# Kernel optimization log

Hardware: AMD Instinct MI355X
Metric: run time of the kernel (lower is better)

Reference implementation:

```python
import jax, jax.numpy as jnp
import numpy as np

KERNEL_MUL = 2.0
KERNEL_NUM = 5


def setup_inputs() -> dict:
    key = jax.random.key(0)
    k1, k2 = jax.random.split(key)
    source = jax.random.normal(k1, (4096, 256), dtype=jnp.float32)
    target = jax.random.normal(k2, (4096, 256), dtype=jnp.float32)
    return {"source": source, "target": target}


def reference(source, target):
    B = source.shape[0]
    total = jnp.concatenate([source, target], axis=0)  # [2N, D]
    n = total.shape[0]
    # Pairwise squared L2 distances via ||a||^2 + ||b||^2 - 2 a.b (same math,
    # avoids the O(n^2 * D) expanded intermediate of the torch code).
    sq = jnp.sum(total * total, axis=-1)  # [2N]
    L2 = sq[:, None] + sq[None, :] - 2.0 * (total @ total.T)  # [2N, 2N]
    L2 = jnp.maximum(L2, 0.0)  # exact distances are non-negative
    # bandwidth uses L2_distance.data in torch -> stop_gradient here
    bandwidth = jax.lax.stop_gradient(jnp.sum(L2)) / (n * n - n)
    bandwidth = bandwidth / (KERNEL_MUL ** (KERNEL_NUM // 2))
    kernels = jnp.zeros_like(L2)
    for i in range(KERNEL_NUM):
        bw = bandwidth * (KERNEL_MUL ** i) + 1e-9
        kernels = kernels + jnp.exp(-L2 / bw)
    xx = jnp.mean(kernels[:B, :B])
    yy = jnp.mean(kernels[B:, B:])
    xy = jnp.mean(kernels[:B, B:])
    yx = jnp.mean(kernels[B:, :B])
    loss = xx + yy - xy - yx  # == mean(XX + YY - XY - YX) since blocks are BxB
    return (loss, jnp.max(L2), xx, yy, xy, yx)
```

## Files before the change

kernel.cpp:

```cpp
#include <hip/hip_runtime.h>
#include <math.h>


constexpr int NTOT  = 8192;
constexpr int BHALF = 4096;
constexpr int DIM   = 256;
constexpr int BM    = 128;

typedef __attribute__((ext_vector_type(8))) short bf16x8;
typedef __attribute__((ext_vector_type(4))) float f32x4;

#define GLOAD_LDS16(gp, lp)                                                      \
    __builtin_amdgcn_global_load_lds(                                            \
        (__attribute__((address_space(1))) const void*)(gp),                     \
        (__attribute__((address_space(3))) void*)(lp), 16, 0, 0)


__device__ __forceinline__ int swz(int row, int byteInRow) {
    return (row * 128 + byteInRow) ^ ((row & 7) << 4);
}

__device__ __forceinline__ unsigned short rne_bf16(float f) {
    unsigned u = __float_as_uint(f);
    return (unsigned short)((u + 0x7fffu + ((u >> 16) & 1u)) >> 16);
}

__global__ __launch_bounds__(256) void prep_kernel(
        const float* __restrict__ src, const float* __restrict__ tgt,
        float* __restrict__ sq, float* __restrict__ colpart,
        unsigned short* __restrict__ hi) {
    __shared__ float cs[4][256];
    const int t = threadIdx.x;
    const int w = t >> 6, l = t & 63;
    const int seg = l >> 4;
    const int b8  = (l * 8) & 127;
    float c0 = 0.f, c1 = 0.f, c2 = 0.f, c3 = 0.f;

#pragma unroll
    for (int it = 0; it < 8; ++it) {
        const int row = blockIdx.x * 32 + w * 8 + it;
        const float* p = (row < BHALF) ? src + (size_t)row * DIM
                                       : tgt + (size_t)(row - BHALF) * DIM;
        float4 v = reinterpret_cast<const float4*>(p)[l];
        float s = v.x * v.x + v.y * v.y + v.z * v.z + v.w * v.w;
#pragma unroll
        for (int off = 32; off; off >>= 1) s += __shfl_down(s, off);
        if (l == 0) sq[row] = s;
        c0 += v.x; c1 += v.y; c2 += v.z; c3 += v.w;

        unsigned hp0 = (unsigned)rne_bf16(v.x) | ((unsigned)rne_bf16(v.y) << 16);
        unsigned hp1 = (unsigned)rne_bf16(v.z) | ((unsigned)rne_bf16(v.w) << 16);
        const size_t byteoff = (size_t)row * 512 + seg * 128 + (b8 ^ ((row & 7) << 4));
        *reinterpret_cast<uint2*>((char*)hi + byteoff) = make_uint2(hp0, hp1);
    }

    cs[w][l * 4 + 0] = c0; cs[w][l * 4 + 1] = c1;
    cs[w][l * 4 + 2] = c2; cs[w][l * 4 + 3] = c3;
    __syncthreads();
    colpart[blockIdx.x * 256 + t] = cs[0][t] + cs[1][t] + cs[2][t] + cs[3][t];
}

__global__ void bw_kernel(const float* __restrict__ sq,
                          const float* __restrict__ colpart,
                          float* __restrict__ bwp) {
    __shared__ double red[256];
    int t = threadIdx.x;
    double s = 0.0;
    for (int i = t; i < NTOT; i += 256) s += (double)sq[i];
    red[t] = s; __syncthreads();
    for (int off = 128; off; off >>= 1) {
        if (t < off) red[t] += red[t + off];
        __syncthreads();
    }
    double S1 = red[0];
    __syncthreads();
    double v = 0.0;
    for (int b = 0; b < 256; ++b) v += (double)colpart[b * 256 + t];
    red[t] = v * v; __syncthreads();
    for (int off = 128; off; off >>= 1) {
        if (t < off) red[t] += red[t + off];
        __syncthreads();
    }
    if (t == 0) {
        double V2 = red[0];
        const double n = (double)NTOT;
        double sumL2 = 2.0 * n * S1 - 2.0 * V2;
        *bwp = (float)(sumL2 / (n * n - n) / 4.0);
    }
}

__global__ __launch_bounds__(256) void gram_kernel(
        const unsigned short* __restrict__ hi,
        const float* __restrict__ sq, const float* __restrict__ bwp,
        double* __restrict__ qsum, int* __restrict__ maxBits) {
    const int tb = blockIdx.x;
    const int id = (tb & 7) * 260 + (tb >> 3);
    int k = 2079 - id;
    int u = (int)((sqrt((double)(8 * k + 1)) - 1.0) * 0.5);
    while ((u + 1) * (u + 2) / 2 <= k) ++u;
    while (u * (u + 1) / 2 > k) --u;
    const int by = 63 - u;
    const int bx = 63 - (k - u * (u + 1) / 2);
    const bool diag = (bx == by);

    __shared__ alignas(16) char ldsA[BM * 128];
    __shared__ alignas(16) char ldsB[BM * 128];
    __shared__ double sred[4];
    __shared__ float  mred[4];

    const int i0 = by * BM;
    const int j0 = bx * BM;
    const char* Ahi = (const char*)hi + (size_t)i0 * 512;
    const char* Bhi = (const char*)hi + (size_t)j0 * 512;

    const int t    = threadIdx.x;
    const int lane = t & 63;
    const int w    = t >> 6;
    const int wr   = w >> 1;
    const int wc   = w & 1;
    const int lrow = lane & 15;

    f32x4 acc[4][4] = {};

    for (int seg = 0; seg < 4; ++seg) {
#pragma unroll
        for (int it = 0; it < 4; ++it) {
            const int chunk = it * 4 + w;
            const int o     = chunk * 1024 + lane * 16;
            const int row   = o >> 7;
            const size_t srcoff = (size_t)row * 512 + seg * 128 + (o & 127);
            GLOAD_LDS16(Ahi + srcoff, ldsA + chunk * 1024);
            if (!diag) GLOAD_LDS16(Bhi + srcoff, ldsB + chunk * 1024);
        }
        __syncthreads();

        const char* bbuf = diag ? ldsA : ldsB;
#pragma unroll
        for (int ks = 0; ks < 2; ++ks) {
            const int kb = ks * 64 + (lane >> 4) * 16;
            bf16x8 a[4], b[4];
#pragma unroll
            for (int mt = 0; mt < 4; ++mt)
                a[mt] = *reinterpret_cast<const bf16x8*>(
                    ldsA + swz(wr * 64 + mt * 16 + lrow, kb));
#pragma unroll
            for (int nt = 0; nt < 4; ++nt)
                b[nt] = *reinterpret_cast<const bf16x8*>(
                    bbuf + swz(wc * 64 + nt * 16 + lrow, kb));
#pragma unroll
            for (int mt = 0; mt < 4; ++mt)
#pragma unroll
                for (int nt = 0; nt < 4; ++nt)
                    acc[mt][nt] = __builtin_amdgcn_mfma_f32_16x16x32_bf16(
                        a[mt], b[nt], acc[mt][nt], 0, 0, 0);
        }
        __syncthreads();
    }

    const float bw  = *bwp;
    const float ic4 = -1.44269504088896340736f / (bw * 16.0f + 1e-9f);

    float m = 0.0f;
    float ksum = 0.0f;
    const int rbase = i0 + wr * 64 + (lane >> 4) * 4;
    const int cbase = j0 + wc * 64 + lrow;
    float sb[4];
#pragma unroll
    for (int nt = 0; nt < 4; ++nt) sb[nt] = sq[cbase + nt * 16];
#pragma unroll
    for (int mt = 0; mt < 4; ++mt) {
        float sa[4];
#pragma unroll
        for (int r = 0; r < 4; ++r) sa[r] = sq[rbase + mt * 16 + r];
#pragma unroll
        for (int nt = 0; nt < 4; ++nt)
#pragma unroll
            for (int r = 0; r < 4; ++r) {
                float l2 = fmaxf(fmaf(-2.0f, acc[mt][nt][r], sa[r] + sb[nt]), 0.0f);
                m = fmaxf(m, l2);
                float e1  = exp2f(l2 * ic4);
                float e2  = e1 * e1;
                float e4  = e2 * e2;
                float e8  = e4 * e4;
                float e16 = e8 * e8;
                ksum += (e1 + e2) + (e4 + e8) + e16;
            }
    }

    double s = (double)ksum;
#pragma unroll
    for (int off = 32; off; off >>= 1) {
        s += __shfl_down(s, off);
        m  = fmaxf(m, __shfl_down(m, off));
    }
    if ((t & 63) == 0) { sred[w] = s; mred[w] = m; }
    __syncthreads();
    if (t == 0) {
        double st = sred[0] + sred[1] + sred[2] + sred[3];
        float  mt = fmaxf(fmaxf(mred[0], mred[1]), fmaxf(mred[2], mred[3]));
        atomicMax(maxBits, __float_as_int(mt));
        const int q  = (((i0 >= BHALF) ? 2 : 0) | ((j0 >= BHALF) ? 1 : 0));
        const int qT = (((j0 >= BHALF) ? 2 : 0) | ((i0 >= BHALF) ? 1 : 0));
        if (diag) {
            atomicAdd(&qsum[q], st);
        } else if (q == qT) {
            atomicAdd(&qsum[q], 2.0 * st);
        } else {
            atomicAdd(&qsum[q],  st);
            atomicAdd(&qsum[qT], st);
        }
    }
}

__global__ void final_kernel(const double* __restrict__ qsum,
                             const int* __restrict__ maxBits,
                             float* __restrict__ out) {
    const double denom = (double)BHALF * (double)BHALF;
    const double xx = qsum[0] / denom;
    const double xy = qsum[1] / denom;
    const double yx = qsum[2] / denom;
    const double yy = qsum[3] / denom;
    out[0] = (float)(xx + yy - xy - yx);
    out[1] = __int_as_float(*maxBits);
    out[2] = (float)xx;
    out[3] = (float)yy;
    out[4] = (float)xy;
    out[5] = (float)yx;
}

extern "C" void kernel_launch(void* const* d_in, const int* in_sizes, int n_in,
                              void* d_out, int out_size, void* d_ws, size_t ws_size,
                              hipStream_t stream) {
    const float* src = (const float*)d_in[0];
    const float* tgt = (const float*)d_in[1];
    float* out = (float*)d_out;

    double* qsum    = (double*)d_ws;
    int*    maxB    = (int*)   ((char*)d_ws + 32);
    float*  bwp     = (float*) ((char*)d_ws + 36);
    float*  sq      = (float*) ((char*)d_ws + 2112);
    unsigned short* hi = (unsigned short*)((char*)d_ws + 36864);
    float*  colpart = (float*) ((char*)d_ws + 36864 + (size_t)NTOT * DIM * 2);

    hipMemsetAsync(d_ws, 0, 64, stream);

    prep_kernel<<<NTOT / 32, 256, 0, stream>>>(src, tgt, sq, colpart, hi);
    bw_kernel<<<1, 256, 0, stream>>>(sq, colpart, bwp);
    gram_kernel<<<2080, 256, 0, stream>>>(hi, sq, bwp, qsum, maxB);
    final_kernel<<<1, 1, 0, stream>>>(qsum, maxB, out);
}
```

Measured before the change: 158.9 us.

## Fold bandwidth and final reductions into last-block epilogues; double-buffer gram LDS

The separate bandwidth and finalize kernels are removed. The last prep block (found by an atomic counter) computes the bandwidth, and the last gram block writes the outputs, which saves two kernel launches and their serialization gaps. The gram kernel also double-buffers its LDS tiles so the next K segment is loaded while the current one feeds MFMA. The cost is twice the LDS use, which may lower occupancy, plus extra atomics and fences.

```diff
diff --git a/kernel.cpp b/kernel.cpp
--- a/kernel.cpp
+++ b/kernel.cpp
@@ -28,13 +28,18 @@
 __global__ __launch_bounds__(256) void prep_kernel(
         const float* __restrict__ src, const float* __restrict__ tgt,
         float* __restrict__ sq, float* __restrict__ colpart,
-        unsigned short* __restrict__ hi) {
-    __shared__ float cs[4][256];
+        float* __restrict__ sqpart, unsigned short* __restrict__ hi,
+        int* __restrict__ prepCounter, float* __restrict__ bwp) {
+    __shared__ float  cs[4][256];
+    __shared__ float  sblk[256];
+    __shared__ double red[256];
+    __shared__ unsigned lastFlag;
     const int t = threadIdx.x;
     const int w = t >> 6, l = t & 63;
     const int seg = l >> 4;
     const int b8  = (l * 8) & 127;
     float c0 = 0.f, c1 = 0.f, c2 = 0.f, c3 = 0.f;
+    float sqacc = 0.f;
 
 #pragma unroll
     for (int it = 0; it < 8; ++it) {
@@ -43,6 +48,7 @@
                                        : tgt + (size_t)(row - BHALF) * DIM;
         float4 v = reinterpret_cast<const float4*>(p)[l];
         float s = v.x * v.x + v.y * v.y + v.z * v.z + v.w * v.w;
+        sqacc += s;
 #pragma unroll
         for (int off = 32; off; off >>= 1) s += __shfl_down(s, off);
         if (l == 0) sq[row] = s;
@@ -56,43 +62,47 @@
 
     cs[w][l * 4 + 0] = c0; cs[w][l * 4 + 1] = c1;
     cs[w][l * 4 + 2] = c2; cs[w][l * 4 + 3] = c3;
+    sblk[t] = sqacc;
     __syncthreads();
     colpart[blockIdx.x * 256 + t] = cs[0][t] + cs[1][t] + cs[2][t] + cs[3][t];
-}
-
-__global__ void bw_kernel(const float* __restrict__ sq,
-                          const float* __restrict__ colpart,
-                          float* __restrict__ bwp) {
-    __shared__ double red[256];
-    int t = threadIdx.x;
-    double s = 0.0;
-    for (int i = t; i < NTOT; i += 256) s += (double)sq[i];
-    red[t] = s; __syncthreads();
     for (int off = 128; off; off >>= 1) {
-        if (t < off) red[t] += red[t + off];
+        if (t < off) sblk[t] += sblk[t + off];
         __syncthreads();
     }
-    double S1 = red[0];
-    __syncthreads();
-    double v = 0.0;
-    for (int b = 0; b < 256; ++b) v += (double)colpart[b * 256 + t];
-    red[t] = v * v; __syncthreads();
-    for (int off = 128; off; off >>= 1) {
-        if (t < off) red[t] += red[t + off];
-        __syncthreads();
-    }
-    if (t == 0) {
-        double V2 = red[0];
-        const double n = (double)NTOT;
-        double sumL2 = 2.0 * n * S1 - 2.0 * V2;
-        *bwp = (float)(sumL2 / (n * n - n) / 4.0);
+    if (t == 0) sqpart[blockIdx.x] = sblk[0];
+
+    __threadfence();
+    if (t == 0) lastFlag = (atomicAdd(prepCounter, 1) == (NTOT / 32 - 1)) ? 1u : 0u;
+    __syncthreads();
+    if (lastFlag) {
+        __threadfence();
+        double v = 0.0;
+        for (int b = 0; b < 256; ++b) v += (double)colpart[b * 256 + t];
+        red[t] = v * v; __syncthreads();
+        for (int off = 128; off; off >>= 1) {
+            if (t < off) red[t] += red[t + off];
+            __syncthreads();
+        }
+        double V2 = red[0]; __syncthreads();
+        red[t] = (double)sqpart[t]; __syncthreads();
+        for (int off = 128; off; off >>= 1) {
+            if (t < off) red[t] += red[t + off];
+            __syncthreads();
+        }
+        if (t == 0) {
+            double S1 = red[0];
+            const double n = (double)NTOT;
+            double sumL2 = 2.0 * n * S1 - 2.0 * V2;
+            *bwp = (float)(sumL2 / (n * n - n) / 4.0);
+        }
     }
 }
 
 __global__ __launch_bounds__(256) void gram_kernel(
         const unsigned short* __restrict__ hi,
         const float* __restrict__ sq, const float* __restrict__ bwp,
-        double* __restrict__ qsum, int* __restrict__ maxBits) {
+        double* __restrict__ qsum, int* __restrict__ maxBits,
+        int* __restrict__ gramCounter, float* __restrict__ out) {
     const int tb = blockIdx.x;
     const int id = (tb & 7) * 260 + (tb >> 3);
     int k = 2079 - id;
@@ -103,10 +113,11 @@
     const int bx = 63 - (k - u * (u + 1) / 2);
     const bool diag = (bx == by);
 
-    __shared__ alignas(16) char ldsA[BM * 128];
-    __shared__ alignas(16) char ldsB[BM * 128];
+    __shared__ alignas(16) char ldsA[2][BM * 128];
+    __shared__ alignas(16) char ldsB[2][BM * 128];
     __shared__ double sred[4];
     __shared__ float  mred[4];
+    __shared__ unsigned lastFlag;
 
     const int i0 = by * BM;
     const int j0 = bx * BM;
@@ -122,19 +133,26 @@
 
     f32x4 acc[4][4] = {};
 
-    for (int seg = 0; seg < 4; ++seg) {
+    auto STAGE = [&](int seg, int buf) {
 #pragma unroll
         for (int it = 0; it < 4; ++it) {
             const int chunk = it * 4 + w;
             const int o     = chunk * 1024 + lane * 16;
             const int row   = o >> 7;
             const size_t srcoff = (size_t)row * 512 + seg * 128 + (o & 127);
-            GLOAD_LDS16(Ahi + srcoff, ldsA + chunk * 1024);
-            if (!diag) GLOAD_LDS16(Bhi + srcoff, ldsB + chunk * 1024);
-        }
-        __syncthreads();
-
-        const char* bbuf = diag ? ldsA : ldsB;
+            GLOAD_LDS16(Ahi + srcoff, &ldsA[buf][chunk * 1024]);
+            if (!diag) GLOAD_LDS16(Bhi + srcoff, &ldsB[buf][chunk * 1024]);
+        }
+    };
+
+    STAGE(0, 0);
+    __syncthreads();
+
+#pragma unroll
+    for (int seg = 0; seg < 4; ++seg) {
+        if (seg < 3) STAGE(seg + 1, (seg + 1) & 1);
+        const char* abuf = ldsA[seg & 1];
+        const char* bbuf = diag ? ldsA[seg & 1] : ldsB[seg & 1];
 #pragma unroll
         for (int ks = 0; ks < 2; ++ks) {
             const int kb = ks * 64 + (lane >> 4) * 16;
@@ -142,7 +160,7 @@
 #pragma unroll
             for (int mt = 0; mt < 4; ++mt)
                 a[mt] = *reinterpret_cast<const bf16x8*>(
-                    ldsA + swz(wr * 64 + mt * 16 + lrow, kb));
+                    abuf + swz(wr * 64 + mt * 16 + lrow, kb));
 #pragma unroll
             for (int nt = 0; nt < 4; ++nt)
                 b[nt] = *reinterpret_cast<const bf16x8*>(
@@ -209,23 +227,26 @@
             atomicAdd(&qsum[q],  st);
             atomicAdd(&qsum[qT], st);
         }
-    }
-}
-
-__global__ void final_kernel(const double* __restrict__ qsum,
-                             const int* __restrict__ maxBits,
-                             float* __restrict__ out) {
-    const double denom = (double)BHALF * (double)BHALF;
-    const double xx = qsum[0] / denom;
-    const double xy = qsum[1] / denom;
-    const double yx = qsum[2] / denom;
-    const double yy = qsum[3] / denom;
-    out[0] = (float)(xx + yy - xy - yx);
-    out[1] = __int_as_float(*maxBits);
-    out[2] = (float)xx;
-    out[3] = (float)yy;
-    out[4] = (float)xy;
-    out[5] = (float)yx;
+        __threadfence();
+        lastFlag = (atomicAdd(gramCounter, 1) == 2079) ? 1u : 0u;
+    }
+    __syncthreads();
+    if (lastFlag && t == 0) {
+        __threadfence();
+        double xx = atomicAdd(&qsum[0], 0.0);
+        double xy = atomicAdd(&qsum[1], 0.0);
+        double yx = atomicAdd(&qsum[2], 0.0);
+        double yy = atomicAdd(&qsum[3], 0.0);
+        int    mb = atomicMax(maxBits, 0);
+        const double denom = (double)BHALF * (double)BHALF;
+        xx /= denom; xy /= denom; yx /= denom; yy /= denom;
+        out[0] = (float)(xx + yy - xy - yx);
+        out[1] = __int_as_float(mb);
+        out[2] = (float)xx;
+        out[3] = (float)yy;
+        out[4] = (float)xy;
+        out[5] = (float)yx;
+    }
 }
 
 extern "C" void kernel_launch(void* const* d_in, const int* in_sizes, int n_in,
@@ -235,17 +256,19 @@
     const float* tgt = (const float*)d_in[1];
     float* out = (float*)d_out;
 
-    double* qsum    = (double*)d_ws;
-    int*    maxB    = (int*)   ((char*)d_ws + 32);
-    float*  bwp     = (float*) ((char*)d_ws + 36);
-    float*  sq      = (float*) ((char*)d_ws + 2112);
+    double* qsum     = (double*)d_ws;
+    int*    maxB     = (int*)   ((char*)d_ws + 32);
+    float*  bwp      = (float*) ((char*)d_ws + 36);
+    int*    gramCnt  = (int*)   ((char*)d_ws + 40);
+    int*    prepCnt  = (int*)   ((char*)d_ws + 44);
+    float*  sq       = (float*) ((char*)d_ws + 2112);
     unsigned short* hi = (unsigned short*)((char*)d_ws + 36864);
-    float*  colpart = (float*) ((char*)d_ws + 36864 + (size_t)NTOT * DIM * 2);
+    float*  colpart  = (float*) ((char*)d_ws + 36864 + (size_t)NTOT * DIM * 2);
+    float*  sqpart   = (float*) ((char*)d_ws + 36864 + (size_t)NTOT * DIM * 2 + 256 * 256 * 4);
 
     hipMemsetAsync(d_ws, 0, 64, stream);
 
-    prep_kernel<<<NTOT / 32, 256, 0, stream>>>(src, tgt, sq, colpart, hi);
-    bw_kernel<<<1, 256, 0, stream>>>(sq, colpart, bwp);
-    gram_kernel<<<2080, 256, 0, stream>>>(hi, sq, bwp, qsum, maxB);
-    final_kernel<<<1, 1, 0, stream>>>(qsum, maxB, out);
-}
+    prep_kernel<<<NTOT / 32, 256, 0, stream>>>(src, tgt, sq, colpart, sqpart, hi,
+                                               prepCnt, bwp);
+    gram_kernel<<<2080, 256, 0, stream>>>(hi, sq, bwp, qsum, maxB, gramCnt, out);
+}
```

Measured after the change: 198.6 us. 25.0% more time.
